# Kernel optimization log

Hardware: AMD Instinct MI355X
Metric: run time of the kernel (lower is better)

Reference implementation:

```python
import jax, jax.numpy as jnp
import numpy as np

# ---- static configuration (mirrors RPN init + FPN anchor generator) ----
IMG_H = 800; IMG_W = 800
STRIDES = [4, 8, 16, 32, 64]
FEAT_SIZES = [(200, 200), (100, 100), (50, 50), (25, 25), (13, 13)]
SCALES = [32.0, 64.0, 128.0, 256.0, 512.0]
RATIOS = [0.5, 1.0, 2.0]
NUM_ANCHORS_PER_LEVEL = [len(RATIOS) * h * w for h, w in FEAT_SIZES]
A_TOTAL = sum(NUM_ANCHORS_PER_LEVEL)  # 159882
BATCH = 4
PRE_NMS_TOP_N = 1000   # _pre_nms_top_n['testing']
POST_NMS_TOP_N = 1000  # _post_nms_top_n['testing']
NMS_THRESH = 0.7
SCORE_THRESH = 0.0
MIN_SIZE = 0.001
BBOX_XFORM_CLIP = float(np.log(1000.0 / 16.0))  # torchvision BoxCoder clamp


def make_anchors():
    out = []
    for (fh, fw), stride, scale in zip(FEAT_SIZES, STRIDES, SCALES):
        base = np.array([[-scale * np.sqrt(1.0 / ar) / 2, -scale * np.sqrt(ar) / 2,
                          scale * np.sqrt(1.0 / ar) / 2, scale * np.sqrt(ar) / 2]
                         for ar in RATIOS], np.float32)  # [A,4]
        sx = (np.arange(fw, dtype=np.float32) + 0.5) * stride
        sy = (np.arange(fh, dtype=np.float32) + 0.5) * stride
        yy, xx = np.meshgrid(sy, sx, indexing='ij')
        shifts = np.stack([xx, yy, xx, yy], axis=-1).reshape(-1, 1, 4)  # [HW,1,4]
        out.append((shifts + base[None]).reshape(-1, 4))  # (H,W,A) ordering
    return np.concatenate(out, axis=0).astype(np.float32)


def setup_inputs() -> dict:
    key = jax.random.key(0)
    k1, k2 = jax.random.split(key)
    objectness = jax.random.normal(k1, (BATCH, A_TOTAL), jnp.float32)
    pred_bbox_deltas = 0.2 * jax.random.normal(k2, (BATCH, A_TOTAL, 4), jnp.float32)
    anchors = jnp.asarray(make_anchors())
    return {"objectness": objectness, "pred_bbox_deltas": pred_bbox_deltas, "anchors": anchors}


def decode_boxes(deltas, anchors):
    # BoxCoder.decode with weights (1,1,1,1)
    wa = anchors[:, 2] - anchors[:, 0]
    ha = anchors[:, 3] - anchors[:, 1]
    cxa = anchors[:, 0] + 0.5 * wa
    cya = anchors[:, 1] + 0.5 * ha
    dx, dy = deltas[..., 0], deltas[..., 1]
    dw = jnp.minimum(deltas[..., 2], BBOX_XFORM_CLIP)
    dh = jnp.minimum(deltas[..., 3], BBOX_XFORM_CLIP)
    cx = dx * wa + cxa
    cy = dy * ha + cya
    w = jnp.exp(dw) * wa
    h = jnp.exp(dh) * ha
    return jnp.stack([cx - 0.5 * w, cy - 0.5 * h, cx + 0.5 * w, cy + 0.5 * h], axis=-1)


def top_n_idx(obj):
    # _get_top_n_idx: per-level top-k with running offset
    idxs = []
    off = 0
    for n in NUM_ANCHORS_PER_LEVEL:
        k = min(PRE_NMS_TOP_N, n)
        _, ti = jax.lax.top_k(obj[:, off:off + n], k)
        idxs.append(ti + off)
        off += n
    return jnp.concatenate(idxs, axis=1)


def pairwise_iou(b):
    area = (b[:, 2] - b[:, 0]) * (b[:, 3] - b[:, 1])
    lt = jnp.maximum(b[:, None, :2], b[None, :, :2])
    rb = jnp.minimum(b[:, None, 2:], b[None, :, 2:])
    wh = jnp.clip(rb - lt, 0.0)
    inter = wh[..., 0] * wh[..., 1]
    return inter / (area[:, None] + area[None, :] - inter)


def nms_single(boxes, scores, levels):
    # clip_boxes_to_image
    x1 = jnp.clip(boxes[:, 0], 0.0, IMG_W)
    y1 = jnp.clip(boxes[:, 1], 0.0, IMG_H)
    x2 = jnp.clip(boxes[:, 2], 0.0, IMG_W)
    y2 = jnp.clip(boxes[:, 3], 0.0, IMG_H)
    boxes = jnp.stack([x1, y1, x2, y2], axis=-1)
    # remove_small_boxes + score_thresh, expressed as a static mask
    valid = (x2 - x1 >= MIN_SIZE) & (y2 - y1 >= MIN_SIZE) & (scores >= SCORE_THRESH)
    # batched_nms trick: offset boxes per level so cross-level IoU is 0
    max_coord = jnp.max(boxes)
    off = levels.astype(boxes.dtype) * (max_coord + 1.0)
    nb = boxes + off[:, None]
    s = jnp.where(valid, scores, -jnp.inf)
    order = jnp.argsort(-s)
    b = nb[order]
    K = b.shape[0]
    iou = pairwise_iou(b)  # [K,K]
    keep0 = valid[order]
    ar = jnp.arange(K)
    def body(i, keep):
        sup = (iou[i] > NMS_THRESH) & (ar > i)
        return jnp.where(keep[i], keep & ~sup, keep)
    keep = jax.lax.fori_loop(0, K, body, keep0)  # greedy NMS
    kept_scores = jnp.where(keep, s[order], -jnp.inf)
    sel = jnp.argsort(-kept_scores)[:POST_NMS_TOP_N]  # stable: preserves score order
    fvalid = jnp.take(keep, sel)
    fb = jnp.take(boxes[order], sel, axis=0)
    fs = jnp.take(scores[order], sel)
    fb = jnp.where(fvalid[:, None], fb, 0.0)  # pad slots zeroed
    fs = jnp.where(fvalid, fs, 0.0)
    return fb, fs


def reference(objectness, pred_bbox_deltas, anchors):
    proposals = decode_boxes(pred_bbox_deltas, anchors)  # [N, A, 4]
    idx = top_n_idx(objectness)  # [N, K]
    levels = jnp.concatenate([jnp.full((n,), i, jnp.int32)
                              for i, n in enumerate(NUM_ANCHORS_PER_LEVEL)])
    bi = jnp.arange(objectness.shape[0])[:, None]
    sc = jax.nn.sigmoid(objectness[bi, idx])
    lv = levels[idx]
    pr = proposals[bi, idx]
    boxes, scores = jax.vmap(nms_single)(pr, sc, lv)
    return boxes, scores  # [N, POST_NMS_TOP_N, 4], [N, POST_NMS_TOP_N]
```

## Files before the change

kernel.cpp:

```cpp
#include <hip/hip_runtime.h>
#include <math.h>

#define BATCH 4
#define A_TOTAL 159882
#define K_TOT 4507
#define N_WORDS 71
#define POST_N 1000

#define OFF_SEL      0u
#define OFF_SKEY     72192u
#define OFF_BOXES    216576u
#define OFF_SCORE    505088u
#define OFF_MAXC     577280u
#define OFF_BOXESS   577536u
#define OFF_NBS      866048u
#define OFF_SCORES   1154560u
#define OFF_SUPINIT  1226752u
#define OFF_MASK     1229056u

__device__ const int d_LVL_N[5]   = {120000, 30000, 7500, 1875, 507};
__device__ const int d_LVL_OFF[5] = {0, 120000, 150000, 157500, 159375};
__device__ const int d_LVL_K[5]   = {1000, 1000, 1000, 1000, 507};
__device__ const int d_CAT_OFF[5] = {0, 1000, 2000, 3000, 4000};

__device__ __forceinline__ float fadd_(float a, float b) { return __fadd_rn(a, b); }
__device__ __forceinline__ float fsub_(float a, float b) { return __fadd_rn(a, -b); }
__device__ __forceinline__ float fmul_(float a, float b) { return __fmul_rn(a, b); }

__device__ __forceinline__ unsigned flipf(float f) {
  unsigned u = __float_as_uint(f);
  return (u & 0x80000000u) ? ~u : (u | 0x80000000u);
}

__device__ __forceinline__ unsigned long long readlane64(unsigned long long v, int l) {
  unsigned lo = (unsigned)__builtin_amdgcn_readlane((int)(unsigned)(v & 0xffffffffull), l);
  unsigned hi = (unsigned)__builtin_amdgcn_readlane((int)(unsigned)(v >> 32), l);
  return ((unsigned long long)hi << 32) | (unsigned long long)lo;
}

__device__ void suffix_and_find(unsigned* hist, unsigned kcur,
                                unsigned* s_bucket, unsigned* s_knew, int tid) {
  for (int off = 1; off < 2048; off <<= 1) {
    unsigned v0 = hist[tid] + ((tid + off) < 2048 ? hist[tid + off] : 0u);
    unsigned v1 = hist[tid + 1024] + ((tid + 1024 + off) < 2048 ? hist[tid + 1024 + off] : 0u);
    __syncthreads();
    hist[tid] = v0; hist[tid + 1024] = v1;
    __syncthreads();
  }
  for (int q = 0; q < 2; ++q) {
    int idx = tid + q * 1024;
    unsigned s0 = hist[idx];
    unsigned s1 = (idx + 1 < 2048) ? hist[idx + 1] : 0u;
    if (s0 >= kcur && s1 < kcur) { *s_bucket = (unsigned)idx; *s_knew = kcur - s1; }
  }
  __syncthreads();
}

__global__ __launch_bounds__(1024) void topk_kernel(const float* __restrict__ obj,
                                                    int* __restrict__ selAnchor) {
  __shared__ unsigned hist[2048];
  __shared__ unsigned long long buf[2048];
  __shared__ unsigned s_bucket, s_knew, s_cnt;
  const int tid = threadIdx.x;
  const int bid = blockIdx.x;
  const int b = bid / 5, l = bid % 5;
  const int n = d_LVL_N[l];
  const int aoff = d_LVL_OFF[l];
  const unsigned kk = (unsigned)d_LVL_K[l];
  const float* src = obj + (size_t)b * A_TOTAL + aoff;

  hist[tid] = 0; hist[tid + 1024] = 0;
  __syncthreads();
  for (int i = tid; i < n; i += 1024) atomicAdd(&hist[flipf(src[i]) >> 21], 1u);
  __syncthreads();
  suffix_and_find(hist, kk, &s_bucket, &s_knew, tid);
  unsigned B1 = s_bucket, k2 = s_knew;
  __syncthreads();

  hist[tid] = 0; hist[tid + 1024] = 0;
  __syncthreads();
  for (int i = tid; i < n; i += 1024) {
    unsigned u = flipf(src[i]);
    if ((u >> 21) == B1) atomicAdd(&hist[(u >> 10) & 2047u], 1u);
  }
  __syncthreads();
  suffix_and_find(hist, k2, &s_bucket, &s_knew, tid);
  unsigned B2 = s_bucket, k3 = s_knew;
  __syncthreads();

  hist[tid] = 0; hist[tid + 1024] = 0;
  __syncthreads();
  unsigned pfx = (B1 << 11) | B2;
  for (int i = tid; i < n; i += 1024) {
    unsigned u = flipf(src[i]);
    if ((u >> 10) == pfx) atomicAdd(&hist[u & 1023u], 1u);
  }
  __syncthreads();
  suffix_and_find(hist, k3, &s_bucket, &s_knew, tid);
  unsigned T = (pfx << 10) | s_bucket;

  if (tid == 0) s_cnt = 0;
  __syncthreads();
  for (int i = tid; i < n; i += 1024) {
    unsigned u = flipf(src[i]);
    if (u >= T) {
      unsigned p = atomicAdd(&s_cnt, 1u);
      if (p < 2048u) buf[p] = ((unsigned long long)u << 32) | (unsigned long long)(~(unsigned)i);
    }
  }
  __syncthreads();
  unsigned cnt = s_cnt; if (cnt > 2048u) cnt = 2048u;
  for (int i = tid; i < 2048; i += 1024) if ((unsigned)i >= cnt) buf[i] = 0ull;
  for (unsigned kq = 2; kq <= 2048; kq <<= 1) {
    for (unsigned j = kq >> 1; j; j >>= 1) {
      __syncthreads();
      unsigned t = (unsigned)tid;
      unsigned i0 = ((t & ~(j - 1)) << 1) | (t & (j - 1));
      unsigned i1 = i0 | j;
      unsigned long long a = buf[i0], c = buf[i1];
      bool up = ((i0 & kq) == 0);
      if (up ? (a < c) : (a > c)) { buf[i0] = c; buf[i1] = a; }
    }
  }
  __syncthreads();
  if ((unsigned)tid < kk) {
    unsigned long long key = buf[tid];
    unsigned lidx = ~(unsigned)(key & 0xffffffffull);
    selAnchor[b * K_TOT + d_CAT_OFF[l] + tid] = aoff + (int)lidx;
  }
}

__global__ __launch_bounds__(512) void decode_kernel(
    const float* __restrict__ obj, const float* __restrict__ deltas,
    const float* __restrict__ anchors, const int* __restrict__ selAnchor,
    unsigned long long* __restrict__ skey, float4* __restrict__ boxes,
    float* __restrict__ score, float* __restrict__ maxc) {
  __shared__ float red[512];
  const int b = blockIdx.x;
  const int tid = threadIdx.x;
  float mymax = 0.0f;
  for (int pos = tid; pos < K_TOT; pos += 512) {
    int a = selAnchor[b * K_TOT + pos];
    float4 an = ((const float4*)anchors)[a];
    float4 dl = ((const float4*)deltas)[(size_t)b * A_TOTAL + a];
    float o = obj[(size_t)b * A_TOTAL + a];
    float wa = fsub_(an.z, an.x), ha = fsub_(an.w, an.y);
    float cxa = fadd_(an.x, fmul_(0.5f, wa));
    float cya = fadd_(an.y, fmul_(0.5f, ha));
    const float CLIP = (float)4.135166556742356;
    float dw = fminf(dl.z, CLIP), dh = fminf(dl.w, CLIP);
    float cx = fadd_(fmul_(dl.x, wa), cxa);
    float cy = fadd_(fmul_(dl.y, ha), cya);
    float w = fmul_((float)exp((double)dw), wa);
    float h = fmul_((float)exp((double)dh), ha);
    float x1 = fsub_(cx, fmul_(0.5f, w));
    float y1 = fsub_(cy, fmul_(0.5f, h));
    float x2 = fadd_(cx, fmul_(0.5f, w));
    float y2 = fadd_(cy, fmul_(0.5f, h));
    x1 = fminf(fmaxf(x1, 0.f), 800.f);
    y1 = fminf(fmaxf(y1, 0.f), 800.f);
    x2 = fminf(fmaxf(x2, 0.f), 800.f);
    y2 = fminf(fmaxf(y2, 0.f), 800.f);
    bool valid = (fsub_(x2, x1) >= 0.001f) && (fsub_(y2, y1) >= 0.001f);
    float s = (float)(1.0 / (1.0 + exp(-(double)o)));
    boxes[b * K_TOT + pos] = make_float4(x1, y1, x2, y2);
    score[b * K_TOT + pos] = s;
    float sm = valid ? s : -INFINITY;
    skey[b * K_TOT + pos] =
        ((unsigned long long)flipf(sm) << 32) | (unsigned long long)(~(unsigned)pos);
    mymax = fmaxf(mymax, fmaxf(fmaxf(x1, y1), fmaxf(x2, y2)));
  }
  red[tid] = mymax;
  __syncthreads();
  for (int s2 = 256; s2 > 0; s2 >>= 1) {
    if (tid < s2) red[tid] = fmaxf(red[tid], red[tid + s2]);
    __syncthreads();
  }
  if (tid == 0) maxc[b] = red[0];
}

__global__ __launch_bounds__(1024) void sort_kernel(
    const unsigned long long* __restrict__ skey, const float4* __restrict__ boxes,
    const float* __restrict__ score, const float* __restrict__ maxc,
    float4* __restrict__ boxesS, float4* __restrict__ nbS,
    float* __restrict__ scoreS, unsigned long long* __restrict__ supInit) {
  __shared__ unsigned long long keys[8192];
  const int b = blockIdx.x;
  const int tid = threadIdx.x;
  for (int t = tid; t < 8192; t += 1024)
    keys[t] = (t < K_TOT) ? skey[b * K_TOT + t] : 0ull;
  for (unsigned kq = 2; kq <= 8192; kq <<= 1) {
    for (unsigned j = kq >> 1; j; j >>= 1) {
      __syncthreads();
      for (unsigned t = (unsigned)tid; t < 4096; t += 1024) {
        unsigned i0 = ((t & ~(j - 1)) << 1) | (t & (j - 1));
        unsigned i1 = i0 | j;
        unsigned long long a = keys[i0], c = keys[i1];
        bool up = ((i0 & kq) == 0);
        if (up ? (a < c) : (a > c)) { keys[i0] = c; keys[i1] = a; }
      }
    }
  }
  __syncthreads();
  float mc1 = fadd_(maxc[b], 1.0f);
  for (int t = tid; t < 8192; t += 1024) {
    unsigned long long key = keys[t];
    bool inr = t < K_TOT;
    unsigned pos = ~(unsigned)(key & 0xffffffffull);
    bool valid = inr && ((unsigned)(key >> 32) != 0x007FFFFFu);
    if (inr) {
      float4 bx = boxes[b * K_TOT + pos];
      boxesS[b * K_TOT + t] = bx;
      int lvl = (int)(pos / 1000u);
      float offv = fmul_((float)lvl, mc1);
      nbS[b * K_TOT + t] = make_float4(fadd_(bx.x, offv), fadd_(bx.y, offv),
                                       fadd_(bx.z, offv), fadd_(bx.w, offv));
      scoreS[b * K_TOT + t] = score[b * K_TOT + pos];
    }
    unsigned long long bal = __ballot(valid);
    if (t < N_WORDS * 64 && (threadIdx.x & 63) == 0)
      supInit[b * N_WORDS + (t >> 6)] = ~bal;
  }
}

__global__ __launch_bounds__(64) void mask_kernel(const float4* __restrict__ nbS,
                                                  unsigned long long* __restrict__ mask) {
  const int b = blockIdx.y;
  int rem = blockIdx.x;
  int ib = 0;
  while (rem >= N_WORDS - ib) { rem -= (N_WORDS - ib); ++ib; }
  const int jb = ib + rem;
  __shared__ float4 jbox[64];
  __shared__ float jarea[64];
  const int lane = threadIdx.x;
  const int j0 = jb * 64;
  {
    int jj = j0 + lane;
    float4 bj = (jj < K_TOT) ? nbS[(size_t)b * K_TOT + jj]
                             : make_float4(-1e30f, -1e30f, -1e30f, -1e30f);
    jbox[lane] = bj;
    jarea[lane] = fmul_(fsub_(bj.z, bj.x), fsub_(bj.w, bj.y));
  }
  __syncthreads();
  const int i = ib * 64 + lane;
  if (i >= K_TOT) return;
  float4 bi = nbS[(size_t)b * K_TOT + i];
  float ai = fmul_(fsub_(bi.z, bi.x), fsub_(bi.w, bi.y));
  unsigned long long bits = 0ull;
  int jmax = K_TOT - j0; if (jmax > 64) jmax = 64;
  for (int q = 0; q < jmax; ++q) {
    int j = j0 + q;
    if (j <= i) continue;
    float4 bj = jbox[q];
    float ltx = fmaxf(bi.x, bj.x), lty = fmaxf(bi.y, bj.y);
    float rbx = fminf(bi.z, bj.z), rby = fminf(bi.w, bj.w);
    float wx = fmaxf(fsub_(rbx, ltx), 0.f), wy = fmaxf(fsub_(rby, lty), 0.f);
    float inter = fmul_(wx, wy);
    float uni = fsub_(fadd_(ai, jarea[q]), inter);
    float iou = inter / uni;
    if (iou > 0.7f) bits |= (1ull << q);
  }
  mask[((size_t)b * K_TOT + i) * N_WORDS + jb] = bits;
}

__global__ __launch_bounds__(64, 1) void scan_kernel(
    const unsigned long long* __restrict__ mask,
    const unsigned long long* __restrict__ supInit,
    const float4* __restrict__ boxesS, const float* __restrict__ scoreS,
    float* __restrict__ out) {
  __shared__ unsigned short keptIdx[POST_N];
  const int b = blockIdx.x;
  const int lane = threadIdx.x;
  const unsigned long long* m = mask + (size_t)b * K_TOT * N_WORDS;
  unsigned long long supA = supInit[b * N_WORDS + lane];
  unsigned long long supB = (lane < N_WORDS - 64) ? supInit[b * N_WORDS + 64 + lane] : ~0ull;
  float4* ob = (float4*)(out + (size_t)b * POST_N * 4);
  float* os = out + 4 * POST_N * 4 + (size_t)b * POST_N;
  const int lane2 = (lane + 64 < N_WORDS) ? (lane + 64) : lane;
  int c = 0;
  unsigned long long rw_cur = (lane < K_TOT) ? m[(size_t)lane * N_WORDS] : 0ull;
  for (int w = 0; w < N_WORDS; ++w) {
    unsigned long long rw_next = 0ull;
    if (w + 1 < N_WORDS) {
      int i1 = (w + 1) * 64 + lane;
      if (i1 < K_TOT) rw_next = m[(size_t)i1 * N_WORDS + (w + 1)];
    }
    unsigned long long v = (w < 64) ? supA : supB;
    int srcl = (w < 64) ? w : (w - 64);
    unsigned long long scur = readlane64(v, srcl);
    unsigned long long avail = ~scur;
    unsigned long long keptm = 0ull;
    while (avail) {
      int t = __builtin_ctzll(avail);
      keptm |= (1ull << t);
      unsigned long long rw = readlane64(rw_cur, t);
      avail &= ~(rw | (1ull << t));
    }
    unsigned long long km = keptm;
    while (km != 0ull && c < POST_N) {
      int t = __builtin_ctzll(km); km &= km - 1ull;
      if (lane == 0) keptIdx[c] = (unsigned short)(w * 64 + t);
      ++c;
    }
    if (c >= POST_N) break;
    if (w + 1 >= N_WORDS) break;
    km = keptm;
    while (km != 0ull) {
      int ts[16];
      unsigned long long vm[16];
#pragma unroll
      for (int q = 0; q < 16; ++q) {
        unsigned long long kms = km ? km : 1ull;
        ts[q] = __builtin_ctzll(kms);
        vm[q] = km ? ~0ull : 0ull;
        km &= km - 1ull;
      }
      unsigned long long dA[16], dB[16];
#pragma unroll
      for (int q = 0; q < 16; ++q) {
        const unsigned long long* row = m + (size_t)(w * 64 + ts[q]) * N_WORDS;
        dA[q] = row[lane];
        dB[q] = row[lane2];
      }
      unsigned long long acc0 = 0ull, acc1 = 0ull;
#pragma unroll
      for (int q = 0; q < 16; ++q) {
        acc0 |= dA[q] & vm[q];
        acc1 |= dB[q] & vm[q];
      }
      supA |= acc0; supB |= acc1;
    }
    rw_cur = rw_next;
  }
  __syncthreads();
  for (int t2 = lane; t2 < c; t2 += 64) {
    int i = keptIdx[t2];
    ob[t2] = boxesS[(size_t)b * K_TOT + i];
    os[t2] = scoreS[(size_t)b * K_TOT + i];
  }
  for (int t2 = c + lane; t2 < POST_N; t2 += 64) {
    ob[t2] = make_float4(0.f, 0.f, 0.f, 0.f);
    os[t2] = 0.f;
  }
}

extern "C" void kernel_launch(void* const* d_in, const int* in_sizes, int n_in,
                              void* d_out, int out_size, void* d_ws, size_t ws_size,
                              hipStream_t stream) {
  const float* obj = (const float*)d_in[0];
  const float* deltas = (const float*)d_in[1];
  const float* anchors = (const float*)d_in[2];
  float* out = (float*)d_out;
  char* ws = (char*)d_ws;

  int* selAnchor = (int*)(ws + OFF_SEL);
  unsigned long long* skey = (unsigned long long*)(ws + OFF_SKEY);
  float4* boxes = (float4*)(ws + OFF_BOXES);
  float* score = (float*)(ws + OFF_SCORE);
  float* maxc = (float*)(ws + OFF_MAXC);
  float4* boxesS = (float4*)(ws + OFF_BOXESS);
  float4* nbS = (float4*)(ws + OFF_NBS);
  float* scoreS = (float*)(ws + OFF_SCORES);
  unsigned long long* supInit = (unsigned long long*)(ws + OFF_SUPINIT);
  unsigned long long* mask = (unsigned long long*)(ws + OFF_MASK);

  hipLaunchKernelGGL(topk_kernel, dim3(BATCH * 5), dim3(1024), 0, stream, obj, selAnchor);
  hipLaunchKernelGGL(decode_kernel, dim3(BATCH), dim3(512), 0, stream,
                     obj, deltas, anchors, selAnchor, skey, boxes, score, maxc);
  hipLaunchKernelGGL(sort_kernel, dim3(BATCH), dim3(1024), 0, stream,
                     skey, boxes, score, maxc, boxesS, nbS, scoreS, supInit);
  hipLaunchKernelGGL(mask_kernel, dim3(N_WORDS * (N_WORDS + 1) / 2, BATCH), dim3(64), 0, stream,
                     nbS, mask);
  hipLaunchKernelGGL(scan_kernel, dim3(BATCH), dim3(64), 0, stream,
                     mask, supInit, boxesS, scoreS, out);
}
```

Measured before the change: 477.7 us.

## Prefetch suppression rows for all candidates before the serial NMS scan

For the first 64 mask words, the NMS scan now issues global loads of the suppression rows for every still-available candidate in the word before the serial greedy loop runs, so memory latency overlaps the readlane chain. After the loop it ORs in only the rows of kept candidates. The second mask half (supB) is no longer updated per word; it is rebuilt once at word 64 from all kept indices with a wave-level OR reduction. Kept-index recording becomes a parallel popcount prefix write instead of a serial loop. The cost is extra loads for candidates that end up suppressed, inline asm with a manual waitcnt, and high register use from the 64-entry arrays.

```diff
diff --git a/kernel.cpp b/kernel.cpp
--- a/kernel.cpp
+++ b/kernel.cpp
@@ -35,6 +35,12 @@
 __device__ __forceinline__ unsigned long long readlane64(unsigned long long v, int l) {
   unsigned lo = (unsigned)__builtin_amdgcn_readlane((int)(unsigned)(v & 0xffffffffull), l);
   unsigned hi = (unsigned)__builtin_amdgcn_readlane((int)(unsigned)(v >> 32), l);
+  return ((unsigned long long)hi << 32) | (unsigned long long)lo;
+}
+
+__device__ __forceinline__ unsigned long long shflxor64(unsigned long long v, int msk) {
+  unsigned lo = __shfl_xor((unsigned)(v & 0xffffffffull), msk, 64);
+  unsigned hi = __shfl_xor((unsigned)(v >> 32), msk, 64);
   return ((unsigned long long)hi << 32) | (unsigned long long)lo;
 }
 
@@ -285,60 +291,120 @@
       int i1 = (w + 1) * 64 + lane;
       if (i1 < K_TOT) rw_next = m[(size_t)i1 * N_WORDS + (w + 1)];
     }
+    if (w == 64) {
+      for (int j = 0; j < N_WORDS - 64; ++j) {
+        unsigned long long acc = 0ull;
+        for (int base = 0; base < c; base += 64) {
+          int k2 = base + lane;
+          unsigned long long v2 = 0ull;
+          if (k2 < c) v2 = m[(size_t)keptIdx[k2] * N_WORDS + 64 + j];
+          acc |= v2;
+        }
+        for (int msk = 32; msk > 0; msk >>= 1) acc |= shflxor64(acc, msk);
+        if (lane == j) supB |= acc;
+      }
+    }
     unsigned long long v = (w < 64) ? supA : supB;
     int srcl = (w < 64) ? w : (w - 64);
     unsigned long long scur = readlane64(v, srcl);
-    unsigned long long avail = ~scur;
+    unsigned long long avail0 = ~scur;
     unsigned long long keptm = 0ull;
-    while (avail) {
-      int t = __builtin_ctzll(avail);
-      keptm |= (1ull << t);
-      unsigned long long rw = readlane64(rw_cur, t);
-      avail &= ~(rw | (1ull << t));
-    }
-    unsigned long long km = keptm;
-    while (km != 0ull && c < POST_N) {
-      int t = __builtin_ctzll(km); km &= km - 1ull;
-      if (lane == 0) keptIdx[c] = (unsigned short)(w * 64 + t);
-      ++c;
-    }
-    if (c >= POST_N) break;
-    if (w + 1 >= N_WORDS) break;
-    km = keptm;
-    while (km != 0ull) {
-      int ts[16];
-      unsigned long long vm[16];
+
+    if (w < 64) {
+      int tq[64];
+      unsigned long long dA[64];
+      unsigned long long av = avail0;
+      if (avail0) {
 #pragma unroll
-      for (int q = 0; q < 16; ++q) {
-        unsigned long long kms = km ? km : 1ull;
-        ts[q] = __builtin_ctzll(kms);
-        vm[q] = km ? ~0ull : 0ull;
-        km &= km - 1ull;
-      }
-      unsigned long long dA[16], dB[16];
+        for (int q = 0; q < 64; ++q) {
+          unsigned long long avq = av ? av : 1ull;
+          tq[q] = __builtin_ctzll(avq);
+          av &= av - 1ull;
+          const unsigned long long* rp = m + (size_t)(w * 64 + tq[q]) * N_WORDS;
+          asm volatile("global_load_dwordx2 %0, %1, off" : "=&v"(dA[q]) : "v"(rp + lane));
+        }
+      }
+      __builtin_amdgcn_sched_barrier(0);
+      unsigned long long avail = avail0;
+      while (avail) {
+        int t = __builtin_ctzll(avail);
+        keptm |= (1ull << t);
+        unsigned long long rw = readlane64(rw_cur, t);
+        avail &= ~(rw | (1ull << t));
+      }
+      int nk = __popcll(keptm);
+      if (keptm) {
+        int pos = c + (int)__popcll(keptm & ((1ull << lane) - 1ull));
+        if (((keptm >> lane) & 1ull) && pos < POST_N)
+          keptIdx[pos] = (unsigned short)(w * 64 + lane);
+      }
+      c += nk;
+      if (c >= POST_N) break;
+      if (avail0) {
+        asm volatile("s_waitcnt vmcnt(0)" ::: "memory");
+        __builtin_amdgcn_sched_barrier(0);
+        unsigned long long acc0 = 0ull;
 #pragma unroll
-      for (int q = 0; q < 16; ++q) {
-        const unsigned long long* row = m + (size_t)(w * 64 + ts[q]) * N_WORDS;
-        dA[q] = row[lane];
-        dB[q] = row[lane2];
-      }
-      unsigned long long acc0 = 0ull, acc1 = 0ull;
+        for (int q = 0; q < 64; ++q) {
+          unsigned long long sel = ((keptm >> tq[q]) & 1ull) ? ~0ull : 0ull;
+          acc0 |= dA[q] & sel;
+        }
+        supA |= acc0;
+      }
+    } else {
+      unsigned long long avail = avail0;
+      while (avail) {
+        int t = __builtin_ctzll(avail);
+        keptm |= (1ull << t);
+        unsigned long long rw = readlane64(rw_cur, t);
+        avail &= ~(rw | (1ull << t));
+      }
+      int nk = __popcll(keptm);
+      if (keptm) {
+        int pos = c + (int)__popcll(keptm & ((1ull << lane) - 1ull));
+        if (((keptm >> lane) & 1ull) && pos < POST_N)
+          keptIdx[pos] = (unsigned short)(w * 64 + lane);
+      }
+      c += nk;
+      if (c >= POST_N) break;
+      if (w + 1 >= N_WORDS) break;
+      unsigned long long km = keptm;
+      while (km != 0ull) {
+        int ts[16];
+        unsigned long long vm[16];
 #pragma unroll
-      for (int q = 0; q < 16; ++q) {
-        acc0 |= dA[q] & vm[q];
-        acc1 |= dB[q] & vm[q];
-      }
-      supA |= acc0; supB |= acc1;
+        for (int q = 0; q < 16; ++q) {
+          unsigned long long kms = km ? km : 1ull;
+          ts[q] = __builtin_ctzll(kms);
+          vm[q] = km ? ~0ull : 0ull;
+          km &= km - 1ull;
+        }
+        unsigned long long dA2[16], dB2[16];
+#pragma unroll
+        for (int q = 0; q < 16; ++q) {
+          const unsigned long long* row = m + (size_t)(w * 64 + ts[q]) * N_WORDS;
+          dA2[q] = row[lane];
+          dB2[q] = row[lane2];
+        }
+        __builtin_amdgcn_sched_barrier(0);
+        unsigned long long acc0 = 0ull, acc1 = 0ull;
+#pragma unroll
+        for (int q = 0; q < 16; ++q) {
+          acc0 |= dA2[q] & vm[q];
+          acc1 |= dB2[q] & vm[q];
+        }
+        supA |= acc0; supB |= acc1;
+      }
     }
     rw_cur = rw_next;
   }
   __syncthreads();
-  for (int t2 = lane; t2 < c; t2 += 64) {
+  for (int t2 = lane; t2 < c && t2 < POST_N; t2 += 64) {
     int i = keptIdx[t2];
     ob[t2] = boxesS[(size_t)b * K_TOT + i];
     os[t2] = scoreS[(size_t)b * K_TOT + i];
   }
-  for (int t2 = c + lane; t2 < POST_N; t2 += 64) {
+  for (int t2 = (c < POST_N ? c : POST_N) + lane; t2 < POST_N; t2 += 64) {
     ob[t2] = make_float4(0.f, 0.f, 0.f, 0.f);
     os[t2] = 0.f;
   }
```

Measured after the change: 423.8 us. 11.3% less time.
